# Performance work log

Measured on AMD Instinct MI355X. Metric: run time of the kernel, lower is better.

Reference implementation:

```python
import jax, jax.numpy as jnp
import numpy as np

NH = 8  # num_heads
T_SOFTMAX = 1.0


def _ln(x, s, b, eps=1e-5):
    m = x.mean(-1, keepdims=True)
    v = ((x - m) ** 2).mean(-1, keepdims=True)
    return (x - m) / jnp.sqrt(v + eps) * s + b


def _encoder(x, qkv_w, qkv_b, out_w, out_b, ln1_s, ln1_b, w1, b1, w2, b2, ln2_s, ln2_b):
    # PyTorch nn.TransformerEncoder (post-norm, ReLU FFN, dropout=0)
    B, N, H = x.shape
    dh = H // NH
    scale = 1.0 / np.sqrt(dh)

    def heads(t):
        return t.reshape(B, N, NH, dh).transpose(0, 2, 1, 3)  # [B,h,N,dh]

    for l in range(qkv_w.shape[0]):
        qkv = x @ qkv_w[l] + qkv_b[l]
        q, k, v = jnp.split(qkv, 3, axis=-1)
        att = jax.nn.softmax(jnp.einsum('bhqd,bhkd->bhqk', heads(q), heads(k)) * scale, axis=-1)
        o = jnp.einsum('bhqk,bhkd->bhqd', att, heads(v)).transpose(0, 2, 1, 3).reshape(B, N, H)
        x = _ln(x + (o @ out_w[l] + out_b[l]), ln1_s[l], ln1_b[l])
        f = jax.nn.relu(x @ w1[l] + b1[l]) @ w2[l] + b2[l]
        x = _ln(x + f, ln2_s[l], ln2_b[l])
    return x


def _route(x, demand2, capacity, gumbel):
    # Batched, fused version of the per-batch python decode loop.
    # Sampling uses the Gumbel-max trick: argmax(scores/T + g) ~ Categorical(softmax(scores/T)).
    B, N, H = x.shape
    ar = jnp.arange(N)

    def step(carry, g):
        cur, visited, cap, lp = carry
        feas = (~visited) & (demand2 <= cap[:, None])          # [B,N]
        active = jnp.any(feas, axis=-1)                        # [B]
        cur_emb = jnp.take_along_axis(x, cur[:, None, None], axis=1)[:, 0, :]  # [B,H]
        scores = jnp.einsum('bh,bnh->bn', cur_emb, x) / T_SOFTMAX
        masked = jnp.where(feas, scores, -1e9)
        logp = jax.nn.log_softmax(masked, axis=-1)
        choice = jnp.argmax(masked + g, axis=-1)               # sampled feasible node
        clp = jnp.take_along_axis(logp, choice[:, None], axis=1)[:, 0]
        cur2 = jnp.where(active, choice, cur)
        lp2 = lp + jnp.where(active, clp, 0.0)
        visited2 = visited | ((ar[None, :] == choice[:, None]) & active[:, None])
        dsel = jnp.take_along_axis(demand2, choice[:, None], axis=1)[:, 0]
        cap2 = cap - jnp.where(active, dsel, 0.0)
        return (cur2, visited2, cap2, lp2), jnp.where(active, choice, 0)

    init = (jnp.zeros((B,), jnp.int32),
            jnp.broadcast_to(ar[None, :] == 0, (B, N)),
            capacity,
            jnp.zeros((B,), x.dtype))
    (_, _, _, lp), nodes = jax.lax.scan(step, init, gumbel)
    route = jnp.concatenate([jnp.zeros((1, B), nodes.dtype), nodes], axis=0).T  # [B, n_steps]
    return route, lp


def setup_inputs() -> dict:
    key = jax.random.key(0)
    ks = jax.random.split(key, 12)
    B, N, H, L = 512, 100, 256, 3
    F = 2 * H
    s = 0.05
    node_feats = jax.random.normal(ks[0], (B * N, 3), jnp.float32)
    demand = jax.random.uniform(ks[1], (B, N), jnp.float32).at[:, 0].set(0.0).reshape(-1)
    capacity = jnp.full((B,), 30.0, jnp.float32)
    u = jax.random.uniform(ks[2], (199, B, N), jnp.float32, 1e-6, 1.0 - 1e-6)
    gumbel = -jnp.log(-jnp.log(u))
    return {
        'node_feats': node_feats,
        'demand': demand,
        'capacity': capacity,
        'gumbel': gumbel,
        'W_node': jax.random.normal(ks[3], (3, H), jnp.float32) * s,
        'b_node': jnp.zeros((H,), jnp.float32),
        'qkv_w': jax.random.normal(ks[4], (L, H, 3 * H), jnp.float32) * s,
        'qkv_b': jnp.zeros((L, 3 * H), jnp.float32),
        'out_w': jax.random.normal(ks[5], (L, H, H), jnp.float32) * s,
        'out_b': jnp.zeros((L, H), jnp.float32),
        'ln1_s': jnp.ones((L, H), jnp.float32),
        'ln1_b': jnp.zeros((L, H), jnp.float32),
        'w1': jax.random.normal(ks[6], (L, H, F), jnp.float32) * s,
        'b1': jnp.zeros((L, F), jnp.float32),
        'w2': jax.random.normal(ks[7], (L, F, H), jnp.float32) * s,
        'b2': jnp.zeros((L, H), jnp.float32),
        'ln2_s': jnp.ones((L, H), jnp.float32),
        'ln2_b': jnp.zeros((L, H), jnp.float32),
        'n_steps': 200,
    }


def reference(node_feats, demand, capacity, gumbel, W_node, b_node, qkv_w, qkv_b,
              out_w, out_b, ln1_s, ln1_b, w1, b1, w2, b2, ln2_s, ln2_b, n_steps):
    B = capacity.shape[0]
    N = node_feats.shape[0] // B
    x = (node_feats @ W_node + b_node).reshape(B, N, -1)
    x = _encoder(x, qkv_w, qkv_b, out_w, out_b, ln1_s, ln1_b, w1, b1, w2, b2, ln2_s, ln2_b)
    route, log_probs = _route(x, demand.reshape(B, N), capacity, gumbel)
    return route, log_probs
```

## Files before the change

kernel.cpp:

```cpp
#include <hip/hip_runtime.h>
#include <math.h>
#include <stdint.h>

constexpr int BATCH  = 512;
constexpr int NNODE  = 100;
constexpr int HDIM   = 256;
constexpr int NHEAD  = 8;
constexpr int DHEAD  = 32;
constexpr int NLAYER = 3;
constexpr int FDIM   = 512;
constexpr int MTOK   = BATCH * NNODE;
constexpr int RLEN   = 200;

typedef unsigned short u16;
typedef unsigned int   u32;
typedef __attribute__((ext_vector_type(8))) short bf16x8;
typedef __attribute__((ext_vector_type(4))) float f32x4;

static __device__ __forceinline__ float wave_sum(float v) {
#pragma unroll
    for (int o = 32; o; o >>= 1) v += __shfl_xor(v, o);
    return v;
}
static __device__ __forceinline__ float wave_max(float v) {
#pragma unroll
    for (int o = 32; o; o >>= 1) v = fmaxf(v, __shfl_xor(v, o));
    return v;
}

static __device__ __forceinline__ u16 f2bf(float f) {
    u32 u = __float_as_uint(f);
    u += 0x7FFFu + ((u >> 16) & 1u);
    return (u16)(u >> 16);
}
static __device__ __forceinline__ float bf2f(u16 h) {
    return __uint_as_float(((u32)h) << 16);
}
static __device__ __forceinline__ u32 pk2(u16 a, u16 b) { return (u32)a | ((u32)b << 16); }

static __device__ __forceinline__ void split_store8(const float* v, u16* ph, u16* pl) {
    u16 h[8], l[8];
#pragma unroll
    for (int j = 0; j < 8; ++j) {
        h[j] = f2bf(v[j]);
        l[j] = f2bf(v[j] - bf2f(h[j]));
    }
    uint4 uh = make_uint4(pk2(h[0], h[1]), pk2(h[2], h[3]), pk2(h[4], h[5]), pk2(h[6], h[7]));
    uint4 ul = make_uint4(pk2(l[0], l[1]), pk2(l[2], l[3]), pk2(l[4], l[5]), pk2(l[6], l[7]));
    *reinterpret_cast<uint4*>(ph) = uh;
    *reinterpret_cast<uint4*>(pl) = ul;
}

__global__ void k_embed(const float* __restrict__ nf, const float* __restrict__ W,
                        const float* __restrict__ bias, float* __restrict__ x) {
    int idx = blockIdx.x * 256 + threadIdx.x;
    int row = idx >> 8;
    int col = idx & 255;
    float a0 = nf[row * 3 + 0], a1 = nf[row * 3 + 1], a2 = nf[row * 3 + 2];
    x[idx] = fmaf(a0, W[col], fmaf(a1, W[256 + col], fmaf(a2, W[512 + col], bias[col])));
}

template<int KSIZE, int NSIZE, bool RELU, bool RES>
__global__ __launch_bounds__(256) void k_mfma(const float* __restrict__ A, int lda,
                                              const float* __restrict__ W,
                                              const float* __restrict__ bias,
                                              const float* __restrict__ res,
                                              float* __restrict__ C) {
    __shared__ u16 Ash[128][40];
    __shared__ u16 Asl[128][40];
    __shared__ u16 Bsh[128][40];
    __shared__ u16 Bsl[128][40];
    const int t    = threadIdx.x;
    const int lane = t & 63, wv = t >> 6;
    const int wr   = wv >> 1, wc = wv & 1;
    const int m0   = blockIdx.y * 128, n0 = blockIdx.x * 128;
    const int sr   = t >> 1;
    const int kh   = (t & 1) * 16;
    const int lr   = lane & 15, ks = (lane >> 4) * 8;

    f32x4 acc[4][4] = {};

    for (int kc = 0; kc < KSIZE; kc += 32) {
        float av[16];
        const float* ap = &A[(size_t)(m0 + sr) * lda + kc + kh];
#pragma unroll
        for (int j = 0; j < 4; ++j) {
            float4 v = *reinterpret_cast<const float4*>(ap + 4 * j);
            av[4 * j + 0] = v.x; av[4 * j + 1] = v.y;
            av[4 * j + 2] = v.z; av[4 * j + 3] = v.w;
        }
        float wvv[16];
        const float* wp = &W[(size_t)(kc + kh) * NSIZE + n0 + sr];
#pragma unroll
        for (int j = 0; j < 16; ++j) wvv[j] = wp[(size_t)j * NSIZE];

        __syncthreads();
        split_store8(av,     &Ash[sr][kh],     &Asl[sr][kh]);
        split_store8(av + 8, &Ash[sr][kh + 8], &Asl[sr][kh + 8]);
        split_store8(wvv,     &Bsh[sr][kh],     &Bsl[sr][kh]);
        split_store8(wvv + 8, &Bsh[sr][kh + 8], &Bsl[sr][kh + 8]);
        __syncthreads();

        bf16x8 afh[4], afl[4], bfh[4], bfl[4];
#pragma unroll
        for (int i = 0; i < 4; ++i) {
            afh[i] = *reinterpret_cast<const bf16x8*>(&Ash[wr * 64 + i * 16 + lr][ks]);
            afl[i] = *reinterpret_cast<const bf16x8*>(&Asl[wr * 64 + i * 16 + lr][ks]);
            bfh[i] = *reinterpret_cast<const bf16x8*>(&Bsh[wc * 64 + i * 16 + lr][ks]);
            bfl[i] = *reinterpret_cast<const bf16x8*>(&Bsl[wc * 64 + i * 16 + lr][ks]);
        }
#pragma unroll
        for (int mi = 0; mi < 4; ++mi)
#pragma unroll
        for (int ni = 0; ni < 4; ++ni) {
            acc[mi][ni] = __builtin_amdgcn_mfma_f32_16x16x32_bf16(afh[mi], bfh[ni], acc[mi][ni], 0, 0, 0);
            acc[mi][ni] = __builtin_amdgcn_mfma_f32_16x16x32_bf16(afh[mi], bfl[ni], acc[mi][ni], 0, 0, 0);
            acc[mi][ni] = __builtin_amdgcn_mfma_f32_16x16x32_bf16(afl[mi], bfh[ni], acc[mi][ni], 0, 0, 0);
        }
    }

#pragma unroll
    for (int ni = 0; ni < 4; ++ni) {
        const int col = n0 + wc * 64 + ni * 16 + lr;
        const float bb = bias[col];
#pragma unroll
        for (int mi = 0; mi < 4; ++mi) {
            const int row0 = m0 + wr * 64 + mi * 16 + (lane >> 4) * 4;
#pragma unroll
            for (int q = 0; q < 4; ++q) {
                size_t off = (size_t)(row0 + q) * NSIZE + col;
                float o = acc[mi][ni][q] + bb;
                if constexpr (RES) o += res[off];
                if constexpr (RELU) o = fmaxf(o, 0.f);
                C[off] = o;
            }
        }
    }
}

static __device__ __forceinline__ float dot32(const float* __restrict__ q,
                                              const float* __restrict__ k) {
    float a = 0.f, b = 0.f;
#pragma unroll
    for (int d = 0; d < 32; d += 2) {
        a = fmaf(q[d],     k[d],     a);
        b = fmaf(q[d + 1], k[d + 1], b);
    }
    return a + b;
}

__global__ __launch_bounds__(64) void k_attn(const float* __restrict__ qkv,
                                             float* __restrict__ out) {
    __shared__ alignas(16) float ks[NNODE * 32];
    __shared__ alignas(16) float vs[NNODE * 32];
    const int b    = blockIdx.x >> 3;
    const int h    = blockIdx.x & 7;
    const int lane = threadIdx.x;
    const float* __restrict__ base = qkv + (size_t)b * NNODE * 768 + h * DHEAD;

    for (int idx = lane; idx < NNODE * 8; idx += 64) {
        int j = idx >> 3, c = idx & 7;
        float4 kv = *reinterpret_cast<const float4*>(base + (size_t)j * 768 + 256 + c * 4);
        float4 vv = *reinterpret_cast<const float4*>(base + (size_t)j * 768 + 512 + c * 4);
        *reinterpret_cast<float4*>(&ks[j * 32 + c * 4]) = kv;
        *reinterpret_cast<float4*>(&vs[j * 32 + c * 4]) = vv;
    }
    __syncthreads();

    const int  i1   = lane;
    const bool has2 = lane < (NNODE - 64);
    const int  i2   = has2 ? lane + 64 : 0;

    float q1[32], q2[32];
    {
        const float* p1 = base + (size_t)i1 * 768;
        const float* p2 = base + (size_t)i2 * 768;
#pragma unroll
        for (int c = 0; c < 8; ++c) {
            float4 a = *reinterpret_cast<const float4*>(p1 + c * 4);
            float4 e = *reinterpret_cast<const float4*>(p2 + c * 4);
            q1[4 * c + 0] = a.x; q1[4 * c + 1] = a.y; q1[4 * c + 2] = a.z; q1[4 * c + 3] = a.w;
            q2[4 * c + 0] = e.x; q2[4 * c + 1] = e.y; q2[4 * c + 2] = e.z; q2[4 * c + 3] = e.w;
        }
    }
    constexpr float scale = 0.17677669529663687f;

    float m1 = -INFINITY, m2 = -INFINITY;
    for (int j = 0; j < NNODE; ++j) {
        const float* kp = &ks[j * 32];
        float kk[32];
#pragma unroll
        for (int c = 0; c < 8; ++c) {
            float4 kv = *reinterpret_cast<const float4*>(kp + c * 4);
            kk[4 * c + 0] = kv.x; kk[4 * c + 1] = kv.y; kk[4 * c + 2] = kv.z; kk[4 * c + 3] = kv.w;
        }
        m1 = fmaxf(m1, dot32(q1, kk) * scale);
        m2 = fmaxf(m2, dot32(q2, kk) * scale);
    }

    float l1 = 0.f, l2 = 0.f;
    float o1[32] = {}, o2[32] = {};
    for (int j = 0; j < NNODE; ++j) {
        const float* kp = &ks[j * 32];
        const float* vp = &vs[j * 32];
        float kk[32];
#pragma unroll
        for (int c = 0; c < 8; ++c) {
            float4 kv = *reinterpret_cast<const float4*>(kp + c * 4);
            kk[4 * c + 0] = kv.x; kk[4 * c + 1] = kv.y; kk[4 * c + 2] = kv.z; kk[4 * c + 3] = kv.w;
        }
        float s1 = dot32(q1, kk) * scale;
        float s2 = dot32(q2, kk) * scale;
        float p1 = __expf(s1 - m1);
        float p2 = __expf(s2 - m2);
        l1 += p1;
        l2 += p2;
#pragma unroll
        for (int c = 0; c < 8; ++c) {
            float4 vv = *reinterpret_cast<const float4*>(vp + c * 4);
            o1[4 * c + 0] = fmaf(p1, vv.x, o1[4 * c + 0]);
            o1[4 * c + 1] = fmaf(p1, vv.y, o1[4 * c + 1]);
            o1[4 * c + 2] = fmaf(p1, vv.z, o1[4 * c + 2]);
            o1[4 * c + 3] = fmaf(p1, vv.w, o1[4 * c + 3]);
            o2[4 * c + 0] = fmaf(p2, vv.x, o2[4 * c + 0]);
            o2[4 * c + 1] = fmaf(p2, vv.y, o2[4 * c + 1]);
            o2[4 * c + 2] = fmaf(p2, vv.z, o2[4 * c + 2]);
            o2[4 * c + 3] = fmaf(p2, vv.w, o2[4 * c + 3]);
        }
    }

    const float inv1 = 1.f / l1;
    float* op1 = out + ((size_t)b * NNODE + i1) * 768 + h * DHEAD;
#pragma unroll
    for (int c = 0; c < 8; ++c) {
        float4 w = make_float4(o1[4 * c + 0] * inv1, o1[4 * c + 1] * inv1,
                               o1[4 * c + 2] * inv1, o1[4 * c + 3] * inv1);
        *reinterpret_cast<float4*>(op1 + c * 4) = w;
    }
    if (has2) {
        const float inv2 = 1.f / l2;
        float* op2 = out + ((size_t)b * NNODE + i2) * 768 + h * DHEAD;
#pragma unroll
        for (int c = 0; c < 8; ++c) {
            float4 w = make_float4(o2[4 * c + 0] * inv2, o2[4 * c + 1] * inv2,
                                   o2[4 * c + 2] * inv2, o2[4 * c + 3] * inv2);
            *reinterpret_cast<float4*>(op2 + c * 4) = w;
        }
    }
}

__global__ __launch_bounds__(256) void k_ln(float* __restrict__ x, const float* __restrict__ sc,
                                            const float* __restrict__ bp) {
    const int row = blockIdx.x * 4 + (threadIdx.x >> 6);
    const int lane = threadIdx.x & 63;
    float* rp = &x[(size_t)row * HDIM + lane * 4];
    float4 v = *reinterpret_cast<const float4*>(rp);
    float mean = wave_sum(v.x + v.y + v.z + v.w) * (1.f / 256.f);
    float d0 = v.x - mean, d1 = v.y - mean, d2 = v.z - mean, d3 = v.w - mean;
    float var = wave_sum(d0 * d0 + d1 * d1 + d2 * d2 + d3 * d3) * (1.f / 256.f);
    float inv = 1.f / sqrtf(var + 1e-5f);
    float4 sv = *reinterpret_cast<const float4*>(&sc[lane * 4]);
    float4 bv = *reinterpret_cast<const float4*>(&bp[lane * 4]);
    float4 ov;
    ov.x = fmaf(d0 * inv, sv.x, bv.x);
    ov.y = fmaf(d1 * inv, sv.y, bv.y);
    ov.z = fmaf(d2 * inv, sv.z, bv.z);
    ov.w = fmaf(d3 * inv, sv.w, bv.w);
    *reinterpret_cast<float4*>(rp) = ov;
}

__global__ __launch_bounds__(256) void k_gram(const float* __restrict__ x, float* __restrict__ S) {
    __shared__ alignas(16) float xs[16][128];
    const int b = blockIdx.x;
    const int t = threadIdx.x, tx = t & 15, ty = t >> 4;
    const int li = t >> 1, lko = (t & 1) * 8;
    float acc[8][8] = {};
    for (int kc = 0; kc < HDIM; kc += 16) {
        float va[8] = {0.f, 0.f, 0.f, 0.f, 0.f, 0.f, 0.f, 0.f};
        if (li < NNODE) {
            const float* p = &x[((size_t)b * NNODE + li) * HDIM + kc + lko];
            float4 u0 = *reinterpret_cast<const float4*>(p);
            float4 u1 = *reinterpret_cast<const float4*>(p + 4);
            va[0] = u0.x; va[1] = u0.y; va[2] = u0.z; va[3] = u0.w;
            va[4] = u1.x; va[5] = u1.y; va[6] = u1.z; va[7] = u1.w;
        }
        __syncthreads();
#pragma unroll
        for (int m = 0; m < 8; ++m) xs[lko + m][li] = va[m];
        __syncthreads();
#pragma unroll
        for (int k = 0; k < 16; ++k) {
            float ai[8], bj[8];
#pragma unroll
            for (int a = 0; a < 8; ++a) ai[a] = xs[k][ty + 16 * a];
#pragma unroll
            for (int c = 0; c < 8; ++c) bj[c] = xs[k][tx + 16 * c];
#pragma unroll
            for (int a = 0; a < 8; ++a)
#pragma unroll
                for (int c = 0; c < 8; ++c)
                    acc[a][c] = fmaf(ai[a], bj[c], acc[a][c]);
        }
    }
#pragma unroll
    for (int a = 0; a < 8; ++a) {
        int i = ty + 16 * a;
        if (i < NNODE) {
#pragma unroll
            for (int c = 0; c < 8; ++c) {
                int j = tx + 16 * c;
                if (j < NNODE) S[(size_t)b * NNODE * NNODE + (size_t)i * NNODE + j] = acc[a][c];
            }
        }
    }
}

__global__ __launch_bounds__(64, 1) void k_route(const float* __restrict__ S,
                                                 const float* __restrict__ demand,
                                                 const float* __restrict__ capacity,
                                                 const float* __restrict__ gumbel,
                                                 float* __restrict__ out, int nsteps) {
    __shared__ alignas(16) float Sl[NNODE * NNODE];
    const int b = blockIdx.x;
    const int lane = threadIdx.x;
    const float* Sb = S + (size_t)b * NNODE * NNODE;
    for (int i = lane; i < NNODE * NNODE / 4; i += 64)
        *reinterpret_cast<float4*>(&Sl[i * 4]) = *reinterpret_cast<const float4*>(&Sb[i * 4]);
    __syncthreads();

    const int j1 = lane, j2 = lane + 64;
    const bool v2 = (j2 < NNODE);
    const float d1 = demand[(size_t)b * NNODE + j1];
    const float d2 = v2 ? demand[(size_t)b * NNODE + j2] : 0.f;
    bool vis1 = (j1 == 0), vis2 = false;
    float cap = capacity[b];
    int cur = 0;
    float lp = 0.f;
    float* route = out + (size_t)b * RLEN;
    if (lane == 0) route[0] = 0.f;

    float g1 = gumbel[(size_t)b * NNODE + j1];
    float g2 = v2 ? gumbel[(size_t)b * NNODE + j2] : 0.f;

    for (int s = 0; s < nsteps; ++s) {
        float ng1 = 0.f, ng2 = 0.f;
        if (s + 1 < nsteps) {
            const float* gn = gumbel + ((size_t)(s + 1) * BATCH + b) * NNODE;
            ng1 = gn[j1];
            ng2 = v2 ? gn[j2] : 0.f;
        }
        bool f1 = (!vis1) && (d1 <= cap);
        bool f2 = v2 && (!vis2) && (d2 <= cap);
        if (__ballot(f1 || f2) == 0ULL) {
            if (lane == 0) route[1 + s] = 0.f;
            g1 = ng1; g2 = ng2;
            continue;
        }
        const float* sr = &Sl[cur * NNODE];
        float m1 = f1 ? sr[j1] : -1e9f;
        float m2 = f2 ? sr[j2] : -1e9f;
        float k1 = m1 + g1;
        float k2 = v2 ? (m2 + g2) : -INFINITY;
        float bk; int bi;
        if (k1 >= k2) { bk = k1; bi = j1; } else { bk = k2; bi = j2; }
#pragma unroll
        for (int off = 32; off; off >>= 1) {
            float ok = __shfl_xor(bk, off);
            int   oi = __shfl_xor(bi, off);
            if (ok > bk || (ok == bk && oi < bi)) { bk = ok; bi = oi; }
        }
        const int choice = bi;
        float mx = wave_max(fmaxf(m1, v2 ? m2 : -1e9f));
        float e = __expf(m1 - mx) + (v2 ? __expf(m2 - mx) : 0.f);
        e = wave_sum(e);
        float msel = __shfl((choice < 64) ? m1 : m2, choice & 63);
        float dsel = __shfl((choice < 64) ? d1 : d2, choice & 63);
        lp += msel - mx - __logf(e);
        if (j1 == choice) vis1 = true;
        if (j2 == choice) vis2 = true;
        cap -= dsel;
        cur = choice;
        if (lane == 0) route[1 + s] = (float)choice;
        g1 = ng1; g2 = ng2;
    }
    if (lane == 0) out[(size_t)BATCH * RLEN + b] = lp;
}

extern "C" void kernel_launch(void* const* d_in, const int* in_sizes, int n_in,
                              void* d_out, int out_size, void* d_ws, size_t ws_size,
                              hipStream_t stream) {
    const float* node_feats = (const float*)d_in[0];
    const float* demand     = (const float*)d_in[1];
    const float* capacity   = (const float*)d_in[2];
    const float* gumbel     = (const float*)d_in[3];
    const float* W_node     = (const float*)d_in[4];
    const float* b_node     = (const float*)d_in[5];
    const float* qkv_w      = (const float*)d_in[6];
    const float* qkv_b      = (const float*)d_in[7];
    const float* out_w      = (const float*)d_in[8];
    const float* out_b      = (const float*)d_in[9];
    const float* ln1_s      = (const float*)d_in[10];
    const float* ln1_b      = (const float*)d_in[11];
    const float* w1         = (const float*)d_in[12];
    const float* b1         = (const float*)d_in[13];
    const float* w2         = (const float*)d_in[14];
    const float* b2         = (const float*)d_in[15];
    const float* ln2_s      = (const float*)d_in[16];
    const float* ln2_b      = (const float*)d_in[17];
    const int gsteps = in_sizes[3] / (BATCH * NNODE);

    float* x    = (float*)d_ws;
    float* buf1 = x + (size_t)MTOK * HDIM;
    float* S    = buf1;
    float* out  = (float*)d_out;

    k_embed<<<MTOK * HDIM / 256, 256, 0, stream>>>(node_feats, W_node, b_node, x);

    for (int l = 0; l < NLAYER; ++l) {
        k_mfma<256, 768, false, false><<<dim3(6, MTOK / 128), 256, 0, stream>>>(
            x, 256, qkv_w + (size_t)l * 256 * 768, qkv_b + (size_t)l * 768, nullptr, buf1);
        k_attn<<<BATCH * NHEAD, 64, 0, stream>>>(buf1, buf1);
        k_mfma<256, 256, false, true><<<dim3(2, MTOK / 128), 256, 0, stream>>>(
            buf1, 768, out_w + (size_t)l * 256 * 256, out_b + (size_t)l * 256, x, x);
        k_ln<<<MTOK / 4, 256, 0, stream>>>(x, ln1_s + (size_t)l * 256, ln1_b + (size_t)l * 256);
        k_mfma<256, 512, true, false><<<dim3(4, MTOK / 128), 256, 0, stream>>>(
            x, 256, w1 + (size_t)l * 256 * 512, b1 + (size_t)l * 512, nullptr, buf1);
        k_mfma<512, 256, false, true><<<dim3(2, MTOK / 128), 256, 0, stream>>>(
            buf1, 512, w2 + (size_t)l * 512 * 256, b2 + (size_t)l * 256, x, x);
        k_ln<<<MTOK / 4, 256, 0, stream>>>(x, ln2_s + (size_t)l * 256, ln2_b + (size_t)l * 256);
    }

    k_gram<<<BATCH, 256, 0, stream>>>(x, S);
    k_route<<<BATCH, 64, 0, stream>>>(S, demand, capacity, gumbel, out, gsteps);
    (void)n_in; (void)out_size; (void)ws_size;
}
```

Before: 1.758 ms.

## Pre-split and transpose weights to bf16 hi/lo once; fuse route reductions

A new pre-pass kernel converts every layer's weight matrix into transposed bf16 high/low pairs in workspace. The GEMM kernel then loads B tiles as contiguous 16-byte vectors instead of strided scalar fp32 loads followed by per-tile splitting, which removes uncoalesced weight reads and redundant conversion work in every block. The routing step also merges the argmax, max, and sum-exp wave reductions into one shuffle loop that carries the selected logit and demand along. The cost is extra launches and workspace for the split weights.

```diff
diff --git a/kernel.cpp b/kernel.cpp
--- a/kernel.cpp
+++ b/kernel.cpp
@@ -60,9 +60,34 @@
     x[idx] = fmaf(a0, W[col], fmaf(a1, W[256 + col], fmaf(a2, W[512 + col], bias[col])));
 }
 
+__global__ __launch_bounds__(256) void k_wsplit(const float* __restrict__ W,
+                                                u16* __restrict__ dh, u16* __restrict__ dl,
+                                                int K, int N) {
+    const int id = blockIdx.x * 256 + threadIdx.x;
+    const int l  = blockIdx.y;
+    if (id >= N * (K / 8)) return;
+    const int n  = id % N;
+    const int k0 = (id / N) * 8;
+    const float* src = W + (size_t)l * K * N;
+    u16* ph = dh + (size_t)l * N * K + (size_t)n * K + k0;
+    u16* pl = dl + (size_t)l * N * K + (size_t)n * K + k0;
+    u16 h[8], lo[8];
+#pragma unroll
+    for (int j = 0; j < 8; ++j) {
+        float f = src[(size_t)(k0 + j) * N + n];
+        h[j]  = f2bf(f);
+        lo[j] = f2bf(f - bf2f(h[j]));
+    }
+    *reinterpret_cast<uint4*>(ph) = make_uint4(pk2(h[0], h[1]), pk2(h[2], h[3]),
+                                               pk2(h[4], h[5]), pk2(h[6], h[7]));
+    *reinterpret_cast<uint4*>(pl) = make_uint4(pk2(lo[0], lo[1]), pk2(lo[2], lo[3]),
+                                               pk2(lo[4], lo[5]), pk2(lo[6], lo[7]));
+}
+
 template<int KSIZE, int NSIZE, bool RELU, bool RES>
 __global__ __launch_bounds__(256) void k_mfma(const float* __restrict__ A, int lda,
-                                              const float* __restrict__ W,
+                                              const u16* __restrict__ WhT,
+                                              const u16* __restrict__ WlT,
                                               const float* __restrict__ bias,
                                               const float* __restrict__ res,
                                               float* __restrict__ C) {
@@ -89,16 +114,20 @@
             av[4 * j + 0] = v.x; av[4 * j + 1] = v.y;
             av[4 * j + 2] = v.z; av[4 * j + 3] = v.w;
         }
-        float wvv[16];
-        const float* wp = &W[(size_t)(kc + kh) * NSIZE + n0 + sr];
-#pragma unroll
-        for (int j = 0; j < 16; ++j) wvv[j] = wp[(size_t)j * NSIZE];
+        const u16* wph = &WhT[(size_t)(n0 + sr) * KSIZE + kc + kh];
+        const u16* wpl = &WlT[(size_t)(n0 + sr) * KSIZE + kc + kh];
+        uint4 bh0 = *reinterpret_cast<const uint4*>(wph);
+        uint4 bh1 = *reinterpret_cast<const uint4*>(wph + 8);
+        uint4 bl0 = *reinterpret_cast<const uint4*>(wpl);
+        uint4 bl1 = *reinterpret_cast<const uint4*>(wpl + 8);
 
         __syncthreads();
         split_store8(av,     &Ash[sr][kh],     &Asl[sr][kh]);
         split_store8(av + 8, &Ash[sr][kh + 8], &Asl[sr][kh + 8]);
-        split_store8(wvv,     &Bsh[sr][kh],     &Bsl[sr][kh]);
-        split_store8(wvv + 8, &Bsh[sr][kh + 8], &Bsl[sr][kh + 8]);
+        *reinterpret_cast<uint4*>(&Bsh[sr][kh])     = bh0;
+        *reinterpret_cast<uint4*>(&Bsh[sr][kh + 8]) = bh1;
+        *reinterpret_cast<uint4*>(&Bsl[sr][kh])     = bl0;
+        *reinterpret_cast<uint4*>(&Bsl[sr][kh + 8]) = bl1;
         __syncthreads();
 
         bf16x8 afh[4], afl[4], bfh[4], bfl[4];
@@ -361,21 +390,29 @@
         float m2 = f2 ? sr[j2] : -1e9f;
         float k1 = m1 + g1;
         float k2 = v2 ? (m2 + g2) : -INFINITY;
-        float bk; int bi;
-        if (k1 >= k2) { bk = k1; bi = j1; } else { bk = k2; bi = j2; }
+        float key, msel, dsel;
+        int idx;
+        if (k1 >= k2) { key = k1; idx = j1; msel = m1; dsel = d1; }
+        else          { key = k2; idx = j2; msel = m2; dsel = d2; }
+        float m = fmaxf(m1, m2);
+        float sum = __expf(m1 - m) + (v2 ? __expf(m2 - m) : 0.f);
 #pragma unroll
         for (int off = 32; off; off >>= 1) {
-            float ok = __shfl_xor(bk, off);
-            int   oi = __shfl_xor(bi, off);
-            if (ok > bk || (ok == bk && oi < bi)) { bk = ok; bi = oi; }
-        }
-        const int choice = bi;
-        float mx = wave_max(fmaxf(m1, v2 ? m2 : -1e9f));
-        float e = __expf(m1 - mx) + (v2 ? __expf(m2 - mx) : 0.f);
-        e = wave_sum(e);
-        float msel = __shfl((choice < 64) ? m1 : m2, choice & 63);
-        float dsel = __shfl((choice < 64) ? d1 : d2, choice & 63);
-        lp += msel - mx - __logf(e);
+            float key2  = __shfl_xor(key, off);
+            int   idx2  = __shfl_xor(idx, off);
+            float msel2 = __shfl_xor(msel, off);
+            float dsel2 = __shfl_xor(dsel, off);
+            float mm2   = __shfl_xor(m, off);
+            float ss2   = __shfl_xor(sum, off);
+            if (key2 > key || (key2 == key && idx2 < idx)) {
+                key = key2; idx = idx2; msel = msel2; dsel = dsel2;
+            }
+            float mn = fmaxf(m, mm2);
+            sum = sum * __expf(m - mn) + ss2 * __expf(mm2 - mn);
+            m = mn;
+        }
+        const int choice = idx;
+        lp += msel - m - __logf(sum);
         if (j1 == choice) vis1 = true;
         if (j2 == choice) vis2 = true;
         cap -= dsel;
@@ -412,21 +449,38 @@
     float* x    = (float*)d_ws;
     float* buf1 = x + (size_t)MTOK * HDIM;
     float* S    = buf1;
-    float* out  = (float*)d_out;
+    u16* qkvTh = (u16*)(buf1 + (size_t)MTOK * 768);
+    u16* qkvTl = qkvTh + (size_t)3 * 768 * 256;
+    u16* prjTh = qkvTl + (size_t)3 * 768 * 256;
+    u16* prjTl = prjTh + (size_t)3 * 256 * 256;
+    u16* f1Th  = prjTl + (size_t)3 * 256 * 256;
+    u16* f1Tl  = f1Th  + (size_t)3 * 512 * 256;
+    u16* f2Th  = f1Tl  + (size_t)3 * 512 * 256;
+    u16* f2Tl  = f2Th  + (size_t)3 * 256 * 512;
+    float* out = (float*)d_out;
+
+    k_wsplit<<<dim3((768 * 32 + 255) / 256, 3), 256, 0, stream>>>(qkv_w, qkvTh, qkvTl, 256, 768);
+    k_wsplit<<<dim3((256 * 32 + 255) / 256, 3), 256, 0, stream>>>(out_w, prjTh, prjTl, 256, 256);
+    k_wsplit<<<dim3((512 * 32 + 255) / 256, 3), 256, 0, stream>>>(w1, f1Th, f1Tl, 256, 512);
+    k_wsplit<<<dim3((256 * 64 + 255) / 256, 3), 256, 0, stream>>>(w2, f2Th, f2Tl, 512, 256);
 
     k_embed<<<MTOK * HDIM / 256, 256, 0, stream>>>(node_feats, W_node, b_node, x);
 
     for (int l = 0; l < NLAYER; ++l) {
         k_mfma<256, 768, false, false><<<dim3(6, MTOK / 128), 256, 0, stream>>>(
-            x, 256, qkv_w + (size_t)l * 256 * 768, qkv_b + (size_t)l * 768, nullptr, buf1);
+            x, 256, qkvTh + (size_t)l * 768 * 256, qkvTl + (size_t)l * 768 * 256,
+            qkv_b + (size_t)l * 768, nullptr, buf1);
         k_attn<<<BATCH * NHEAD, 64, 0, stream>>>(buf1, buf1);
         k_mfma<256, 256, false, true><<<dim3(2, MTOK / 128), 256, 0, stream>>>(
-            buf1, 768, out_w + (size_t)l * 256 * 256, out_b + (size_t)l * 256, x, x);
+            buf1, 768, prjTh + (size_t)l * 256 * 256, prjTl + (size_t)l * 256 * 256,
+            out_b + (size_t)l * 256, x, x);
         k_ln<<<MTOK / 4, 256, 0, stream>>>(x, ln1_s + (size_t)l * 256, ln1_b + (size_t)l * 256);
         k_mfma<256, 512, true, false><<<dim3(4, MTOK / 128), 256, 0, stream>>>(
-            x, 256, w1 + (size_t)l * 256 * 512, b1 + (size_t)l * 512, nullptr, buf1);
+            x, 256, f1Th + (size_t)l * 512 * 256, f1Tl + (size_t)l * 512 * 256,
+            b1 + (size_t)l * 512, nullptr, buf1);
         k_mfma<512, 256, false, true><<<dim3(2, MTOK / 128), 256, 0, stream>>>(
-            buf1, 512, w2 + (size_t)l * 512 * 256, b2 + (size_t)l * 256, x, x);
+            buf1, 512, f2Th + (size_t)l * 256 * 512, f2Tl + (size_t)l * 256 * 512,
+            b2 + (size_t)l * 256, x, x);
         k_ln<<<MTOK / 4, 256, 0, stream>>>(x, ln2_s + (size_t)l * 256, ln2_b + (size_t)l * 256);
     }
 
```

Measured after the change: 1.648 ms. 6.3% less time.
